# Optimization experiments

Hardware: AMD Instinct MI355X
Metric: run time of the kernel (lower is better)

The kernel has to match this reference:

```python
import jax, jax.numpy as jnp
import numpy as np

EPS = 1e-5
NUM_GRAPHS = 512


def _glorot(key, shape):
    lim = float(np.sqrt(6.0 / (shape[0] + shape[1])))
    return jax.random.uniform(key, shape, jnp.float32, -lim, lim)


def setup_inputs() -> dict:
    key = jax.random.key(0)
    ks = jax.random.split(key, 20)
    N, E, F0 = 50000, 800000, 64
    x = jax.random.normal(ks[0], (N, F0), jnp.float32)
    edge_index = jax.random.randint(ks[1], (2, E), 0, N, jnp.int64)
    batch = jnp.sort(jax.random.randint(ks[2], (N,), 0, NUM_GRAPHS, jnp.int64))
    dims = [(F0, 128), (128, 64), (64, 32)]
    p = {}
    for i, (di, do) in enumerate(dims, start=1):
        p[f"W{i}l"] = _glorot(ks[3 * i], (di, do))
        p[f"b{i}"] = jnp.zeros((do,), jnp.float32)
        p[f"W{i}r"] = _glorot(ks[3 * i + 1], (di, do))
        p[f"g{i}"] = jnp.ones((do,), jnp.float32)
        p[f"be{i}"] = jnp.zeros((do,), jnp.float32)
    p["Wf1"] = _glorot(ks[13], (32, 128)); p["bf1"] = jnp.zeros((128,), jnp.float32)
    p["Wf2"] = _glorot(ks[14], (128, 64)); p["bf2"] = jnp.zeros((64,), jnp.float32)
    p["Wf3"] = _glorot(ks[15], (64, 2)); p["bf3"] = jnp.zeros((2,), jnp.float32)
    return {"x": x, "edge_index": edge_index, "batch": batch, **p}


def _sage(x, src, dst, Wl, bl, Wr, n):
    # mean-aggregate neighbor features (gather from src, scatter-mean to dst)
    agg = jax.ops.segment_sum(x[src], dst, num_segments=n)
    cnt = jax.ops.segment_sum(jnp.ones((src.shape[0],), x.dtype), dst, num_segments=n)
    mean = agg / jnp.maximum(cnt, 1.0)[:, None]
    return mean @ Wl + bl + x @ Wr


def _bn(x, g, b):
    mu = jnp.mean(x, axis=0)
    var = jnp.mean((x - mu) ** 2, axis=0)  # biased var, torch training mode
    return (x - mu) * jax.lax.rsqrt(var + EPS) * g + b


def reference(x, edge_index, batch,
              W1l, b1, W1r, g1, be1,
              W2l, b2, W2r, g2, be2,
              W3l, b3, W3r, g3, be3,
              Wf1, bf1, Wf2, bf2, Wf3, bf3):
    n = x.shape[0]
    src, dst = edge_index[0], edge_index[1]
    h = _bn(jax.nn.relu(_sage(x, src, dst, W1l, b1, W1r, n)), g1, be1)
    h = _bn(jax.nn.relu(_sage(h, src, dst, W2l, b2, W2r, n)), g2, be2)
    h = _bn(jax.nn.relu(_sage(h, src, dst, W3l, b3, W3r, n)), g3, be3)
    pooled = jax.ops.segment_sum(h, batch, num_segments=NUM_GRAPHS)  # [G, 32]
    cr = jax.nn.relu(pooled @ Wf1 + bf1)  # dropout = identity (eval)
    cr = jax.nn.relu(cr @ Wf2 + bf2)
    cr = cr @ Wf3 + bf3
    return cr.reshape(-1, 2)
```

## Files before the change

### kernel.cpp

```cpp
#include <hip/hip_runtime.h>
#include <hip/hip_bf16.h>

#define EPSBN 1e-5f
#define NGRAPH 512
#define SCAN_NB 128

typedef __attribute__((ext_vector_type(8))) short bf16x8;
typedef __attribute__((ext_vector_type(4))) float f32x4;

__device__ inline short f2bf(float f) {
    unsigned u = __builtin_bit_cast(unsigned, f);
    u += 0x7fffu + ((u >> 16) & 1u);
    return (short)(u >> 16);
}
__device__ inline float bf2f(short s) {
    unsigned u = ((unsigned)(unsigned short)s) << 16;
    return __builtin_bit_cast(float, u);
}
__device__ inline int xcd_id() {
    int x;
    asm volatile("s_getreg_b32 %0, hwreg(HW_REG_XCC_ID, 0, 4)" : "=s"(x));
    return x & 7;
}

__global__ void __launch_bounds__(256) k_hist8(
    const int* __restrict__ dst, int* __restrict__ hist8, int E, int Npad)
{
    int* h = hist8 + xcd_id() * Npad;
    const int stride = gridDim.x * 256;
    for (int e = blockIdx.x * 256 + threadIdx.x; e < E; e += stride)
        atomicAdd(&h[dst[e]], 1);
}

__global__ void __launch_bounds__(256) k_scan1(
    const int* __restrict__ hist8, int* __restrict__ blocksum, int N, int Npad)
{
    __shared__ int red[256];
    const int C = (N + SCAN_NB - 1) / SCAN_NB;
    const int b = blockIdx.x, t = threadIdx.x;
    const int lo = b * C, hi = min(lo + C, N);
    int s = 0;
    for (int i = lo + t; i < hi; i += 256) {
        int v = 0;
        #pragma unroll
        for (int c = 0; c < 8; c++) v += hist8[c * Npad + i];
        s += v;
    }
    red[t] = s;
    __syncthreads();
    for (int off = 128; off; off >>= 1) {
        if (t < off) red[t] += red[t + off];
        __syncthreads();
    }
    if (t == 0) blocksum[b] = red[0];
}

__global__ void __launch_bounds__(256) k_scan3(
    const int* __restrict__ hist8, const int* __restrict__ blocksum,
    int* __restrict__ row_off, int* __restrict__ cursor, int N, int Npad)
{
    __shared__ int red[256];
    __shared__ int boff_s;
    const int C = (N + SCAN_NB - 1) / SCAN_NB;
    const int b = blockIdx.x, t = threadIdx.x;
    const int lo = b * C, hi = min(lo + C, N);
    if (t == 0) {
        int acc = 0;
        for (int i = 0; i < b; i++) acc += blocksum[i];
        boff_s = acc;
        if (b == SCAN_NB - 1) {
            int tot = acc;
            for (int i = b; i < SCAN_NB; i++) tot += blocksum[i];
            row_off[N] = tot;
        }
    }
    const int TC = (C + 255) / 256;
    const int s0 = lo + t * TC;
    const int s1 = min(s0 + TC, hi);
    auto hsum = [&](int i) {
        int v = 0;
        #pragma unroll
        for (int c = 0; c < 8; c++) v += hist8[c * Npad + i];
        return v;
    };
    int s = 0;
    for (int i = s0; i < s1; i++) s += hsum(i);
    red[t] = s;
    __syncthreads();
    for (int off = 1; off < 256; off <<= 1) {
        int u = (t >= off) ? red[t - off] : 0;
        __syncthreads();
        red[t] += u;
        __syncthreads();
    }
    int run = boff_s + red[t] - s;
    for (int i = s0; i < s1; i++) {
        row_off[i] = run;
        cursor[i] = run;
        run += hsum(i);
    }
}

__global__ void __launch_bounds__(256) k_scatter(
    const int* __restrict__ src, const int* __restrict__ dst,
    int* __restrict__ cursor, int* __restrict__ csr, int E)
{
    for (int e = blockIdx.x * 256 + threadIdx.x; e < E; e += gridDim.x * 256) {
        int d = dst[e];
        int p = atomicAdd(&cursor[d], 1);
        csr[p] = src[e];
    }
}

__device__ inline int lbound(const int* __restrict__ a, int n, int v) {
    int lo = 0, hi = n;
    while (lo < hi) {
        int mid = (lo + hi) >> 1;
        if (a[mid] < v) lo = mid + 1; else hi = mid;
    }
    return lo;
}
__global__ void __launch_bounds__(256) k_gcnt_bs(
    const int* __restrict__ batch, float* __restrict__ gcnt, int N)
{
    int g = blockIdx.x * 256 + threadIdx.x;
    if (g < NGRAPH)
        gcnt[g] = (float)(lbound(batch, N, g + 1) - lbound(batch, N, g));
}

template <int F>
__global__ void __launch_bounds__(256) k_gatherb(
    const short* __restrict__ feat, const int* __restrict__ row_off,
    const int* __restrict__ csr, short* __restrict__ aggb, int N)
{
    constexpr int LPR = F / 8;
    constexpr int RPB = 256 / LPR;
    const int lane = threadIdx.x % LPR;
    const int rloc = threadIdx.x / LPR;
    const short* fbase = feat + lane * 8;
    for (int row = blockIdx.x * RPB + rloc; row < N; row += gridDim.x * RPB) {
        const int s0 = row_off[row];
        const int s1 = row_off[row + 1];
        float acc0[8], acc1[8];
        #pragma unroll
        for (int i = 0; i < 8; i++) { acc0[i] = 0.f; acc1[i] = 0.f; }
        int p = s0;
        for (; p + 3 < s1; p += 4) {
            int sA = csr[p], sB = csr[p + 1], sC = csr[p + 2], sD = csr[p + 3];
            bf16x8 va = *(const bf16x8*)&fbase[(long long)sA * F];
            bf16x8 vb = *(const bf16x8*)&fbase[(long long)sB * F];
            bf16x8 vc = *(const bf16x8*)&fbase[(long long)sC * F];
            bf16x8 vd = *(const bf16x8*)&fbase[(long long)sD * F];
            #pragma unroll
            for (int i = 0; i < 8; i++) {
                acc0[i] += bf2f(va[i]) + bf2f(vc[i]);
                acc1[i] += bf2f(vb[i]) + bf2f(vd[i]);
            }
        }
        for (; p < s1; p++) {
            int sA = csr[p];
            bf16x8 va = *(const bf16x8*)&fbase[(long long)sA * F];
            #pragma unroll
            for (int i = 0; i < 8; i++) acc0[i] += bf2f(va[i]);
        }
        short o[8];
        #pragma unroll
        for (int i = 0; i < 8; i++) o[i] = f2bf(acc0[i] + acc1[i]);
        *(bf16x8*)&aggb[(long long)row * F + lane * 8] = *(bf16x8*)o;
    }
}

__global__ void __launch_bounds__(256) k_cvt(
    const float* __restrict__ in, short* __restrict__ out, long long n4)
{
    long long i = (long long)blockIdx.x * 256 + threadIdx.x;
    if (i >= n4) return;
    float4 v = *(const float4*)&in[i * 4];
    short4 o = make_short4(f2bf(v.x), f2bf(v.y), f2bf(v.z), f2bf(v.w));
    *(short4*)&out[i * 4] = o;
}

template <int K, int F, bool AFF>
__global__ void __launch_bounds__(64) k_wprep2(
    const float* __restrict__ Wl, const float* __restrict__ Wr,
    const float* __restrict__ a, const float* __restrict__ c,
    const float* __restrict__ bias,
    short* __restrict__ Wlt, short* __restrict__ Wrt,
    float* __restrict__ cvl, float* __restrict__ cvr)
{
    int j = blockIdx.x * 64 + threadIdx.x;
    const bool second = j >= F;
    const int jj = second ? j - F : j;
    if (jj >= F || j >= 2 * F) return;
    const float* W = second ? Wr : Wl;
    short* Wt = second ? Wrt : Wlt;
    float cv = (second && bias) ? bias[jj] : 0.f;
    for (int k = 0; k < K; k++) {
        float w = W[k * F + jj];
        float aa = 1.f;
        if constexpr (AFF) {
            aa = a[k];
            cv += c[k] * w;
        }
        Wt[jj * K + k] = f2bf(aa * w);
    }
    if (second) cvr[jj] = cv; else cvl[jj] = cv;
}

template <int K, int FOUT, bool DUAL, bool HASBASE, bool FINAL, bool OUTBF16,
          bool POOL>
__global__ void __launch_bounds__(256) k_mgemm(
    const short* __restrict__ A, const short* __restrict__ A2,
    const short* __restrict__ Wt, const short* __restrict__ Wt2,
    const float* __restrict__ cvec, const short* __restrict__ base,
    const int* __restrict__ row_off, void* outv,
    float* __restrict__ s_out, float* __restrict__ q_out,
    const int* __restrict__ batchp, float* __restrict__ praw8, int N)
{
    constexpr int KS = K / 32;
    constexpr int NCT = FOUT / 16;
    const int lane = threadIdx.x & 63;
    const int wid = threadIdx.x >> 6;
    const int g = lane >> 4;
    const int mi = lane & 15;
    const int RT = (N + 15) >> 4;
    const int nw = gridDim.x * 4;
    float* outf = (float*)outv;
    short* outb = (short*)outv;
    float* pr = nullptr;
    if constexpr (POOL) pr = praw8 + (size_t)xcd_id() * NGRAPH * 32;

    float st_s[FINAL ? NCT : 1];
    float st_q[FINAL ? NCT : 1];
    if constexpr (FINAL) {
        #pragma unroll
        for (int ct = 0; ct < NCT; ct++) { st_s[ct] = 0.f; st_q[ct] = 0.f; }
    }

    for (int rt = blockIdx.x * 4 + wid; rt < RT; rt += nw) {
        const int m0 = rt * 16;
        int arow = m0 + mi;
        if (arow >= N) arow = N - 1;

        bf16x8 af[KS];
        bf16x8 af2[DUAL ? KS : 1];
        const short* ap = A + (long long)arow * K;
        #pragma unroll
        for (int s = 0; s < KS; s++)
            af[s] = *(const bf16x8*)(ap + s * 32 + g * 8);
        if constexpr (DUAL) {
            const short* ap2 = A2 + (long long)arow * K;
            #pragma unroll
            for (int s = 0; s < KS; s++)
                af2[s] = *(const bf16x8*)(ap2 + s * 32 + g * 8);
        }

        float invc[4];
        if constexpr (DUAL || HASBASE) {
            #pragma unroll
            for (int r = 0; r < 4; r++) {
                int row = m0 + 4 * g + r;
                int cnt = 1;
                if (row < N) cnt = max(row_off[row + 1] - row_off[row], 1);
                invc[r] = 1.f / (float)cnt;
            }
        }
        int bidx[4];
        if constexpr (POOL) {
            #pragma unroll
            for (int r = 0; r < 4; r++) {
                int row = m0 + 4 * g + r;
                bidx[r] = (row < N) ? batchp[row] : -1;
            }
        }

        #pragma unroll
        for (int ct = 0; ct < NCT; ct++) {
            f32x4 acc = {0.f, 0.f, 0.f, 0.f};
            f32x4 acc2 = {0.f, 0.f, 0.f, 0.f};
            const short* bp = Wt + (long long)(ct * 16 + mi) * K;
            #pragma unroll
            for (int s = 0; s < KS; s++) {
                bf16x8 bf = *(const bf16x8*)(bp + s * 32 + g * 8);
                acc = __builtin_amdgcn_mfma_f32_16x16x32_bf16(af[s], bf, acc, 0, 0, 0);
                if constexpr (DUAL) {
                    bf16x8 bf2 = *(const bf16x8*)(Wt2 + (long long)(ct * 16 + mi) * K + s * 32 + g * 8);
                    acc2 = __builtin_amdgcn_mfma_f32_16x16x32_bf16(af2[s], bf2, acc2, 0, 0, 0);
                }
            }
            float cv = cvec[ct * 16 + mi];
            float sl = 0.f, ql = 0.f;
            #pragma unroll
            for (int r = 0; r < 4; r++) {
                int row = m0 + 4 * g + r;
                if (row < N) {
                    float v = acc[r] + cv;
                    if constexpr (DUAL) v = fmaf(invc[r], acc2[r], v);
                    if constexpr (HASBASE)
                        v = fmaf(invc[r], bf2f(base[(long long)row * FOUT + ct * 16 + mi]), v);
                    if constexpr (FINAL) v = fmaxf(v, 0.f);
                    if constexpr (POOL) {
                        atomicAdd(&pr[bidx[r] * FOUT + ct * 16 + mi], v);
                    } else if constexpr (OUTBF16) {
                        outb[(long long)row * FOUT + ct * 16 + mi] = f2bf(v);
                    } else {
                        outf[(long long)row * FOUT + ct * 16 + mi] = v;
                    }
                    if constexpr (FINAL) { sl += v; ql += v * v; }
                }
            }
            if constexpr (FINAL) {
                sl += __shfl_xor(sl, 16, 64);
                sl += __shfl_xor(sl, 32, 64);
                ql += __shfl_xor(ql, 16, 64);
                ql += __shfl_xor(ql, 32, 64);
                st_s[ct] += sl;
                st_q[ct] += ql;
            }
        }
    }

    if constexpr (FINAL) {
        __shared__ float redS[4][NCT][16];
        __shared__ float redQ[4][NCT][16];
        if (lane < 16) {
            #pragma unroll
            for (int ct = 0; ct < NCT; ct++) {
                redS[wid][ct][lane] = st_s[ct];
                redQ[wid][ct][lane] = st_q[ct];
            }
        }
        __syncthreads();
        if (wid == 0 && lane < 16) {
            #pragma unroll
            for (int ct = 0; ct < NCT; ct++) {
                float s = redS[0][ct][lane] + redS[1][ct][lane] +
                          redS[2][ct][lane] + redS[3][ct][lane];
                float q = redQ[0][ct][lane] + redQ[1][ct][lane] +
                          redQ[2][ct][lane] + redQ[3][ct][lane];
                atomicAdd(&s_out[ct * 16 + lane], s);
                atomicAdd(&q_out[ct * 16 + lane], q);
            }
        }
    }
}

__global__ void k_finalize(const float* __restrict__ s, const float* __restrict__ q,
                           const float* __restrict__ g, const float* __restrict__ be,
                           float* __restrict__ a, float* __restrict__ c,
                           int F, float invN)
{
    int j = threadIdx.x;
    if (j < F) {
        float mu = s[j] * invN;
        float var = q[j] * invN - mu * mu;
        float aj = g[j] / sqrtf(var + EPSBN);
        a[j] = aj;
        c[j] = be[j] - mu * aj;
    }
}

__global__ void __launch_bounds__(128) k_mlp(
    const float* __restrict__ praw8, const float* __restrict__ a3,
    const float* __restrict__ c3, const float* __restrict__ gcnt,
    const float* __restrict__ Wf1, const float* __restrict__ bf1,
    const float* __restrict__ Wf2, const float* __restrict__ bf2,
    const float* __restrict__ Wf3, const float* __restrict__ bf3,
    float* __restrict__ out)
{
    __shared__ float p[32], h1[128], h2[64];
    int g = blockIdx.x, t = threadIdx.x;
    if (t < 32) {
        float s = 0.f;
        #pragma unroll
        for (int c = 0; c < 8; c++)
            s += praw8[(size_t)c * NGRAPH * 32 + g * 32 + t];
        p[t] = a3[t] * s + gcnt[g] * c3[t];
    }
    __syncthreads();
    {
        float acc = bf1[t];
        #pragma unroll
        for (int k = 0; k < 32; k++) acc += p[k] * Wf1[k * 128 + t];
        h1[t] = fmaxf(acc, 0.f);
    }
    __syncthreads();
    if (t < 64) {
        float acc = bf2[t];
        #pragma unroll
        for (int k = 0; k < 128; k++) acc += h1[k] * Wf2[k * 64 + t];
        h2[t] = fmaxf(acc, 0.f);
    }
    __syncthreads();
    if (t < 2) {
        float acc = bf3[t];
        #pragma unroll
        for (int k = 0; k < 64; k++) acc += h2[k] * Wf3[k * 2 + t];
        out[g * 2 + t] = acc;
    }
}

extern "C" void kernel_launch(void* const* d_in, const int* in_sizes, int n_in,
                              void* d_out, int out_size, void* d_ws, size_t ws_size,
                              hipStream_t stream)
{
    const float* x     = (const float*)d_in[0];
    const int*   ei    = (const int*)d_in[1];
    const int*   batch = (const int*)d_in[2];
    const float* W1l = (const float*)d_in[3];
    const float* b1  = (const float*)d_in[4];
    const float* W1r = (const float*)d_in[5];
    const float* g1  = (const float*)d_in[6];
    const float* be1 = (const float*)d_in[7];
    const float* W2l = (const float*)d_in[8];
    const float* b2  = (const float*)d_in[9];
    const float* W2r = (const float*)d_in[10];
    const float* g2  = (const float*)d_in[11];
    const float* be2 = (const float*)d_in[12];
    const float* W3l = (const float*)d_in[13];
    const float* b3  = (const float*)d_in[14];
    const float* W3r = (const float*)d_in[15];
    const float* g3  = (const float*)d_in[16];
    const float* be3 = (const float*)d_in[17];
    const float* Wf1 = (const float*)d_in[18];
    const float* bf1 = (const float*)d_in[19];
    const float* Wf2 = (const float*)d_in[20];
    const float* bf2 = (const float*)d_in[21];
    const float* Wf3 = (const float*)d_in[22];
    const float* bf3 = (const float*)d_in[23];

    const int N = in_sizes[0] / 64;
    const int E = in_sizes[1] / 2;
    const int Npad = (N + 255) & ~255;
    const int* src = ei;
    const int* dst = ei + E;

    char* ws = (char*)d_ws;
    size_t off = 0;
    auto alloc = [&](size_t bytes) {
        size_t o = off;
        off += (bytes + 511) & ~(size_t)511;
        return o;
    };
    const size_t o_rowoff = alloc((size_t)(N + 1) * 4);
    const size_t o_cursor = alloc((size_t)N * 4);
    const size_t o_bsum   = alloc(SCAN_NB * 4);
    const size_t o_csr    = alloc((size_t)E * 4);
    const size_t o_zoneB  = alloc((size_t)N * 128);
    const size_t o_zoneC  = alloc((size_t)N * 128);
    const size_t o_zoneD  = alloc((size_t)N * 256);
    const size_t o_zoneE  = alloc((size_t)N * 128);
    const size_t o_aff    = alloc(448 * 4);
    const size_t o_cvec   = alloc(512 * 4);
    const size_t o_wt     = alloc((8192 * 4 + 2048 * 2) * 2);
    const size_t o_gcnt   = alloc((size_t)NGRAPH * 4);
    const size_t o_zero0  = off;
    const size_t o_hist8  = alloc((size_t)Npad * 8 * 4);
    const size_t o_stats  = alloc(448 * 4);
    const size_t o_praw8  = alloc((size_t)NGRAPH * 32 * 4 * 8);
    const size_t zero_len = off - o_zero0;
    (void)ws_size;

    int* row_off = (int*)(ws + o_rowoff);
    int* hist8   = (int*)(ws + o_hist8);
    int* cursor  = (int*)(ws + o_cursor);
    int* bsum    = (int*)(ws + o_bsum);
    int* csr     = (int*)(ws + o_csr);
    short* xb   = (short*)(ws + o_zoneB);
    short* y2b  = (short*)(ws + o_zoneB);
    short* aggb = (short*)(ws + o_zoneC);
    short* t2b  = (short*)(ws + o_zoneC);
    short* t1b  = (short*)(ws + o_zoneD);
    short* y3b  = (short*)(ws + o_zoneD);
    short* m2b  = (short*)(ws + o_zoneE);
    short* m3b  = (short*)(ws + o_zoneE);
    float* praw8 = (float*)(ws + o_praw8);
    float* gcnt  = (float*)(ws + o_gcnt);
    float* s1 = (float*)(ws + o_stats);
    float* q1 = s1 + 128;
    float* s2 = q1 + 128;
    float* q2 = s2 + 64;
    float* s3 = q2 + 64;
    float* q3 = s3 + 32;
    float* a1 = (float*)(ws + o_aff);
    float* c1 = a1 + 128;
    float* a2 = c1 + 128;
    float* c2 = a2 + 64;
    float* a3 = c2 + 64;
    float* c3 = a3 + 32;
    float* cv1l = (float*)(ws + o_cvec);
    float* cv1r = cv1l + 128;
    float* cv2l = cv1r + 128;
    float* cv2r = cv2l + 64;
    float* cv3l = cv2r + 64;
    float* cv3r = cv3l + 32;
    short* W1l_t = (short*)(ws + o_wt);
    short* W1r_t = W1l_t + 8192;
    short* W2l_t = W1r_t + 8192;
    short* W2r_t = W2l_t + 8192;
    short* W3l_t = W2r_t + 8192;
    short* W3r_t = W3l_t + 2048;

    const float invN = 1.0f / (float)N;
    const int MG = 512;

    hipMemsetAsync(ws + o_zero0, 0, zero_len, stream);

    k_hist8<<<2048, 256, 0, stream>>>(dst, hist8, E, Npad);
    k_scan1<<<SCAN_NB, 256, 0, stream>>>(hist8, bsum, N, Npad);
    k_scan3<<<SCAN_NB, 256, 0, stream>>>(hist8, bsum, row_off, cursor, N, Npad);
    k_scatter<<<2048, 256, 0, stream>>>(src, dst, cursor, csr, E);
    k_gcnt_bs<<<2, 256, 0, stream>>>(batch, gcnt, N);

    k_cvt<<<(int)(((long long)N * 16 + 255) / 256), 256, 0, stream>>>(
        x, xb, (long long)N * 16);
    k_wprep2<64, 128, false><<<4, 64, 0, stream>>>(
        W1l, W1r, nullptr, nullptr, b1, W1l_t, W1r_t, cv1l, cv1r);

    k_gatherb<64><<<(N + 31) / 32, 256, 0, stream>>>(
        xb, row_off, csr, aggb, N);
    k_mgemm<64, 128, true, false, true, true, false><<<MG, 256, 0, stream>>>(
        xb, aggb, W1r_t, W1l_t, cv1r, nullptr, row_off, t1b, s1, q1,
        nullptr, nullptr, N);
    k_finalize<<<1, 128, 0, stream>>>(s1, q1, g1, be1, a1, c1, 128, invN);

    k_wprep2<128, 64, true><<<2, 64, 0, stream>>>(
        W2l, W2r, a1, c1, b2, W2l_t, W2r_t, cv2l, cv2r);
    k_mgemm<128, 64, false, false, false, true, false><<<MG, 256, 0, stream>>>(
        t1b, nullptr, W2l_t, nullptr, cv2l, nullptr, row_off, y2b,
        nullptr, nullptr, nullptr, nullptr, N);
    k_gatherb<64><<<(N + 31) / 32, 256, 0, stream>>>(
        y2b, row_off, csr, m2b, N);
    k_mgemm<128, 64, false, true, true, true, false><<<MG, 256, 0, stream>>>(
        t1b, nullptr, W2r_t, nullptr, cv2r, m2b, row_off, t2b, s2, q2,
        nullptr, nullptr, N);
    k_finalize<<<1, 64, 0, stream>>>(s2, q2, g2, be2, a2, c2, 64, invN);

    k_wprep2<64, 32, true><<<1, 64, 0, stream>>>(
        W3l, W3r, a2, c2, b3, W3l_t, W3r_t, cv3l, cv3r);
    k_mgemm<64, 32, false, false, false, true, false><<<MG, 256, 0, stream>>>(
        t2b, nullptr, W3l_t, nullptr, cv3l, nullptr, row_off, y3b,
        nullptr, nullptr, nullptr, nullptr, N);
    k_gatherb<32><<<(N + 63) / 64, 256, 0, stream>>>(
        y3b, row_off, csr, m3b, N);
    k_mgemm<64, 32, false, true, true, false, true><<<MG, 256, 0, stream>>>(
        t2b, nullptr, W3r_t, nullptr, cv3r, m3b, row_off, nullptr, s3, q3,
        batch, praw8, N);
    k_finalize<<<1, 32, 0, stream>>>(s3, q3, g3, be3, a3, c3, 32, invN);

    k_mlp<<<NGRAPH, 128, 0, stream>>>(praw8, a3, c3, gcnt,
                                      Wf1, bf1, Wf2, bf2, Wf3, bf3,
                                      (float*)d_out);
}
```

Before: 294.4 us.

## Gather with one wavefront per row, splitting neighbors across lanes

Replaces the per-row thread-group gather, where a few lanes walk all of a row's neighbors serially, with one wavefront per destination row. Lanes are split into neighbor slots times feature chunks, and partial sums are combined with xor shuffles. This adds memory-level parallelism per row and is meant to cut the serial latency chain on rows with many edges (average degree about 16). In exchange it adds shuffle reduction cost, leaves lanes idle on low-degree rows, launches many more small blocks, and has only one lane group write the result.

```diff
diff --git a/kernel.cpp b/kernel.cpp
--- a/kernel.cpp
+++ b/kernel.cpp
@@ -129,44 +129,42 @@
 }
 
 template <int F>
-__global__ void __launch_bounds__(256) k_gatherb(
+__global__ void __launch_bounds__(256) k_gatherw(
     const short* __restrict__ feat, const int* __restrict__ row_off,
     const int* __restrict__ csr, short* __restrict__ aggb, int N)
 {
-    constexpr int LPR = F / 8;
-    constexpr int RPB = 256 / LPR;
-    const int lane = threadIdx.x % LPR;
-    const int rloc = threadIdx.x / LPR;
-    const short* fbase = feat + lane * 8;
-    for (int row = blockIdx.x * RPB + rloc; row < N; row += gridDim.x * RPB) {
-        const int s0 = row_off[row];
-        const int s1 = row_off[row + 1];
-        float acc0[8], acc1[8];
-        #pragma unroll
-        for (int i = 0; i < 8; i++) { acc0[i] = 0.f; acc1[i] = 0.f; }
-        int p = s0;
-        for (; p + 3 < s1; p += 4) {
-            int sA = csr[p], sB = csr[p + 1], sC = csr[p + 2], sD = csr[p + 3];
-            bf16x8 va = *(const bf16x8*)&fbase[(long long)sA * F];
-            bf16x8 vb = *(const bf16x8*)&fbase[(long long)sB * F];
-            bf16x8 vc = *(const bf16x8*)&fbase[(long long)sC * F];
-            bf16x8 vd = *(const bf16x8*)&fbase[(long long)sD * F];
-            #pragma unroll
-            for (int i = 0; i < 8; i++) {
-                acc0[i] += bf2f(va[i]) + bf2f(vc[i]);
-                acc1[i] += bf2f(vb[i]) + bf2f(vd[i]);
-            }
-        }
-        for (; p < s1; p++) {
-            int sA = csr[p];
-            bf16x8 va = *(const bf16x8*)&fbase[(long long)sA * F];
-            #pragma unroll
-            for (int i = 0; i < 8; i++) acc0[i] += bf2f(va[i]);
-        }
+    constexpr int FL = F / 8;
+    constexpr int NB = 64 / FL;
+    const int wid = threadIdx.x >> 6;
+    const int lane = threadIdx.x & 63;
+    const int fl = lane % FL;
+    const int nbr = lane / FL;
+    const int row = blockIdx.x * 4 + wid;
+    if (row >= N) return;
+    const int s0 = row_off[row];
+    const int s1 = row_off[row + 1];
+    const short* fbase = feat + fl * 8;
+
+    float acc[8];
+    #pragma unroll
+    for (int i = 0; i < 8; i++) acc[i] = 0.f;
+    for (int p = s0 + nbr; p < s1; p += NB) {
+        int sA = csr[p];
+        bf16x8 va = *(const bf16x8*)&fbase[(long long)sA * F];
+        #pragma unroll
+        for (int i = 0; i < 8; i++) acc[i] += bf2f(va[i]);
+    }
+    #pragma unroll
+    for (int off = FL; off < 64; off <<= 1) {
+        #pragma unroll
+        for (int i = 0; i < 8; i++)
+            acc[i] += __shfl_xor(acc[i], off, 64);
+    }
+    if (nbr == 0) {
         short o[8];
         #pragma unroll
-        for (int i = 0; i < 8; i++) o[i] = f2bf(acc0[i] + acc1[i]);
-        *(bf16x8*)&aggb[(long long)row * F + lane * 8] = *(bf16x8*)o;
+        for (int i = 0; i < 8; i++) o[i] = f2bf(acc[i]);
+        *(bf16x8*)&aggb[(long long)row * F + fl * 8] = *(bf16x8*)o;
     }
 }
 
@@ -503,6 +501,7 @@
 
     const float invN = 1.0f / (float)N;
     const int MG = 512;
+    const int GW = (N + 3) / 4;
 
     hipMemsetAsync(ws + o_zero0, 0, zero_len, stream);
 
@@ -517,8 +516,7 @@
     k_wprep2<64, 128, false><<<4, 64, 0, stream>>>(
         W1l, W1r, nullptr, nullptr, b1, W1l_t, W1r_t, cv1l, cv1r);
 
-    k_gatherb<64><<<(N + 31) / 32, 256, 0, stream>>>(
-        xb, row_off, csr, aggb, N);
+    k_gatherw<64><<<GW, 256, 0, stream>>>(xb, row_off, csr, aggb, N);
     k_mgemm<64, 128, true, false, true, true, false><<<MG, 256, 0, stream>>>(
         xb, aggb, W1r_t, W1l_t, cv1r, nullptr, row_off, t1b, s1, q1,
         nullptr, nullptr, N);
@@ -529,8 +527,7 @@
     k_mgemm<128, 64, false, false, false, true, false><<<MG, 256, 0, stream>>>(
         t1b, nullptr, W2l_t, nullptr, cv2l, nullptr, row_off, y2b,
         nullptr, nullptr, nullptr, nullptr, N);
-    k_gatherb<64><<<(N + 31) / 32, 256, 0, stream>>>(
-        y2b, row_off, csr, m2b, N);
+    k_gatherw<64><<<GW, 256, 0, stream>>>(y2b, row_off, csr, m2b, N);
     k_mgemm<128, 64, false, true, true, true, false><<<MG, 256, 0, stream>>>(
         t1b, nullptr, W2r_t, nullptr, cv2r, m2b, row_off, t2b, s2, q2,
         nullptr, nullptr, N);
@@ -541,8 +538,7 @@
     k_mgemm<64, 32, false, false, false, true, false><<<MG, 256, 0, stream>>>(
         t2b, nullptr, W3l_t, nullptr, cv3l, nullptr, row_off, y3b,
         nullptr, nullptr, nullptr, nullptr, N);
-    k_gatherb<32><<<(N + 63) / 64, 256, 0, stream>>>(
-        y3b, row_off, csr, m3b, N);
+    k_gatherw<32><<<GW, 256, 0, stream>>>(y3b, row_off, csr, m3b, N);
     k_mgemm<64, 32, false, true, true, false, true><<<MG, 256, 0, stream>>>(
         t2b, nullptr, W3r_t, nullptr, cv3r, m3b, row_off, nullptr, s3, q3,
         batch, praw8, N);
```

Result: slower. 317.0 us (+7.7%).
